# Kernel optimization log

Measured on AMD Instinct MI355X. Metric: run time of the kernel, lower is better.

## Reference

```python
import jax, jax.numpy as jnp
import numpy as np

B, C, MX, MY, MZ = 4, 64, 48, 48, 48
A, E = 64, 128  # n_atoms, mol_embed_size
V = MX * MY * MZ


def setup_inputs() -> dict:
    key = jax.random.key(0)
    ks = jax.random.split(key, 12)
    inp = {
        "x": jax.random.normal(ks[0], (B, C, MX, MY, MZ), dtype=jnp.float32),
        "mol_embed": jax.random.normal(ks[1], (B, A, E), dtype=jnp.float32),
        "pos": jax.random.uniform(ks[2], (B, A, 3), dtype=jnp.float32),
        "origin": jnp.zeros((B, 3), dtype=jnp.float32),
        "lattice": jax.random.uniform(ks[3], (B, 3, 3), dtype=jnp.float32) + 0.5,
        "batch_nodes": jax.random.randint(ks[4], (B,), 32, A + 1, dtype=jnp.int32),
        "v_w": jax.random.normal(ks[5], (C, E), dtype=jnp.float32) / np.sqrt(E),
        "v_b": jax.random.normal(ks[6], (C,), dtype=jnp.float32) * 0.01,
        "out_w": jax.random.normal(ks[7], (C, 2 * C), dtype=jnp.float32) / np.sqrt(2 * C),
        "out_b": jax.random.normal(ks[8], (C,), dtype=jnp.float32) * 0.01,
        "conv_w": jax.random.normal(ks[9], (C, C, 3, 3, 3), dtype=jnp.float32) / np.sqrt(C * 27),
        "conv_b": jax.random.normal(ks[10], (C,), dtype=jnp.float32) * 0.01,
    }
    return inp


def _grid_points(o, ldiag):
    # torch.linspace(o, o+l, n) inclusive endpoints -> t = arange(n)/(n-1)
    axes = [o[i] + ldiag[i] * (jnp.arange(n, dtype=jnp.float32) / (n - 1))
            for i, n in enumerate((MX, MY, MZ))]
    gx, gy, gz = jnp.meshgrid(*axes, indexing="ij")
    return jnp.stack([gx, gy, gz], axis=-1).reshape(-1, 3)  # [V,3]


def _forward(x, mol_embed, pos, origin, lattice, batch_nodes,
             v_w, v_b, out_w, out_b, conv_w, conv_b):
    b = x.shape[0]
    ldiag = jnp.diagonal(lattice, axis1=-2, axis2=-1)           # [b,3]
    grid = jax.vmap(_grid_points)(origin, ldiag)                # [b,V,3]
    # pairwise distances via |g|^2 + |p|^2 - 2 g.p (avoids [b,V,A,3])
    g2 = jnp.sum(grid * grid, axis=-1)                          # [b,V]
    p2 = jnp.sum(pos * pos, axis=-1)                            # [b,A]
    gp = jnp.einsum("bvd,bad->bva", grid, pos)                  # [b,V,A]
    d2 = g2[:, :, None] + p2[:, None, :] - 2.0 * gp
    dist = jnp.sqrt(jnp.maximum(d2, 1e-12))
    # ragged mask: atoms >= batch_nodes[i] get -inf score
    valid = jnp.arange(A)[None, None, :] < batch_nodes[:, None, None]
    weight = jnp.where(valid, -dist, -jnp.inf)
    att = jax.nn.softmax(weight, axis=-1)                       # [b,V,A]
    v = mol_embed @ v_w.T + v_b                                 # [b,A,C]
    v = jnp.einsum("bva,bac->bvc", att, v)                      # [b,V,C]
    xv = x.reshape(b, C, V).transpose(0, 2, 1)                  # [b,V,C]
    h = jnp.concatenate([xv, v], axis=-1)                       # [b,V,2C]
    h = jax.nn.relu(h @ out_w.T + out_b)                        # [b,V,C]
    h = h.transpose(0, 2, 1).reshape(b, C, MX, MY, MZ)
    hp = jnp.pad(h, ((0, 0), (0, 0), (1, 1), (1, 1), (1, 1)), mode="wrap")
    conv = jax.lax.conv_general_dilated(
        hp, conv_w, window_strides=(1, 1, 1), padding="VALID",
        dimension_numbers=("NCDHW", "OIDHW", "NCDHW"))
    conv = conv + conv_b[None, :, None, None, None]
    return jax.nn.relu(conv) + x


def reference(x, mol_embed, pos, origin, lattice, batch_nodes,
              v_w, v_b, out_w, out_b, conv_w, conv_b):
    return _forward(x, mol_embed, pos, origin, lattice, batch_nodes,
                    v_w, v_b, out_w, out_b, conv_w, conv_b)
```

## Files before the change

### kernel.cpp

```cpp
#include <hip/hip_runtime.h>

#define NB 4
#define NC 64
#define NV (48*48*48)
#define NA 64
#define NE 128

typedef __attribute__((ext_vector_type(8))) short short8;
typedef __attribute__((ext_vector_type(4))) float f32x4;

static __device__ __forceinline__ ushort f2bf(float f) {
  unsigned u = __float_as_uint(f);
  unsigned r = (u + 0x7FFF + ((u >> 16) & 1)) >> 16;
  return (ushort)r;
}
static __device__ __forceinline__ unsigned pk2bf(float lo, float hi) {
  return (unsigned)f2bf(lo) | ((unsigned)f2bf(hi) << 16);
}

__global__ __launch_bounds__(256) void k_vm(
    const float* __restrict__ me, const float* __restrict__ vw,
    const float* __restrict__ vb, float* __restrict__ vmat) {
  int blk = blockIdx.x;
  int b = blk >> 4, aq = blk & 15;
  int t = threadIdx.x;
  int a = aq * 4 + (t >> 6);
  int c = t & 63;
  const float* mp = me + (size_t)(b * 64 + a) * 128;
  const float* wp = vw + (size_t)c * 128;
  float acc = vb[c];
#pragma unroll 8
  for (int e = 0; e < 128; e += 4) {
    float4 m4 = *(const float4*)(mp + e);
    float4 w4 = *(const float4*)(wp + e);
    acc += m4.x * w4.x + m4.y * w4.y + m4.z * w4.z + m4.w * w4.w;
  }
  vmat[b * 4096 + a * 64 + c] = acc;
}

__global__ __launch_bounds__(256) void k_bct(
    const float* __restrict__ ow, const float* __restrict__ vmat,
    ushort* __restrict__ BcT) {
  __shared__ float VM[64 * 68];
  __shared__ float WV[8 * 68];
  int blk = blockIdx.x;
  int b = blk >> 3, og = blk & 7;
  int t = threadIdx.x;
  for (int i = t; i < 4096; i += 256)
    VM[(i >> 6) * 68 + (i & 63)] = vmat[b * 4096 + i];
  for (int i = t; i < 512; i += 256)
    WV[(i >> 6) * 68 + (i & 63)] = ow[(og * 8 + (i >> 6)) * 128 + 64 + (i & 63)];
  __syncthreads();
  int ol = t >> 5;
  int a0 = (t & 31) * 2;
  int o = og * 8 + ol;
#pragma unroll
  for (int p = 0; p < 2; ++p) {
    int a = a0 + p;
    float acc = 0.f;
#pragma unroll 8
    for (int c = 0; c < 64; c += 4) {
      float4 v4 = *(const float4*)&VM[a * 68 + c];
      float4 w4 = *(const float4*)&WV[ol * 68 + c];
      acc += v4.x * w4.x + v4.y * w4.y + v4.z * w4.z + v4.w * w4.w;
    }
    BcT[b * 8192 + o * 128 + a] = f2bf(acc);
  }
#pragma unroll
  for (int p = 0; p < 2; ++p) {
    int i = t * 2 + p;
    int ol2 = i >> 6, ci = i & 63;
    int o2 = og * 8 + ol2;
    BcT[b * 8192 + o2 * 128 + 64 + ci] = f2bf(ow[o2 * 128 + ci]);
  }
}

__global__ void k_wt(const float* __restrict__ cw, ushort* __restrict__ wbf) {
  int idx = blockIdx.x * 256 + threadIdx.x;
  if (idx >= 27 * 64 * 64) return;
  int off = idx >> 12, r = idx & 4095;
  int kcw = r >> 11, r2 = r & 2047, nt = r2 >> 9, r3 = r2 & 511;
  int ln = r3 >> 3, e = r3 & 7;
  int co = nt * 16 + (ln & 15), ci = kcw * 32 + (ln >> 4) * 8 + e;
  wbf[idx] = f2bf(cw[(co * 64 + ci) * 27 + off]);
}

__global__ __launch_bounds__(256) void k_att2(
    const float* __restrict__ x, const float* __restrict__ pos,
    const float* __restrict__ origin, const float* __restrict__ lattice,
    const int* __restrict__ bnodes, const float* __restrict__ ob,
    const ushort* __restrict__ BcT, ushort* __restrict__ hbf) {
  __shared__ __align__(16) char Ac[32768];
  __shared__ float ps[192];
  __shared__ float sinv[128];
  int t = threadIdx.x;
  int lane = t & 63, wave = t >> 6;
  int b = blockIdx.y;
  int v0 = blockIdx.x * 128;
  int lm = lane & 15, lg = lane >> 4;

  if (t < 192) ps[t] = pos[b * 192 + t];
  __syncthreads();

  int cp = t >> 3;
  int vq = t & 7;
  const float* xa = x + ((size_t)(b * 64 + 2 * cp)) * NV + v0 + vq * 16;
  const float* xb2 = xa + NV;
  float4 fa[4], fb[4];
#pragma unroll
  for (int it = 0; it < 4; ++it) {
    fa[it] = *(const float4*)(xa + it * 4);
    fb[it] = *(const float4*)(xb2 + it * 4);
  }
  short8 Bf[4][4];
  {
    const ushort* bp = BcT + b * 8192 + lm * 128 + lg * 8;
#pragma unroll
    for (int kb = 0; kb < 4; ++kb)
#pragma unroll
      for (int nt = 0; nt < 4; ++nt)
        Bf[kb][nt] = *(const short8*)(bp + nt * 2048 + kb * 32);
  }
  __builtin_amdgcn_sched_barrier(0);

  {
    int v_loc = wave * 32 + (lane & 31);
    int half = lane >> 5;
    int v = v0 + v_loc;
    int ix = v / 2304;
    int rem = v - ix * 2304;
    int iy = rem / 48;
    int iz = rem - iy * 48;
    float gx = origin[b * 3 + 0] + lattice[b * 9 + 0] * (ix * (1.0f / 47.0f));
    float gy = origin[b * 3 + 1] + lattice[b * 9 + 4] * (iy * (1.0f / 47.0f));
    float gz = origin[b * 3 + 2] + lattice[b * 9 + 8] * (iz * (1.0f / 47.0f));
    int na = bnodes[b];
    int vswz = v_loc & 7;
    char* rowp = Ac + v_loc * 256;
    float s = 0.f;
#pragma unroll
    for (int i = 0; i < 32; i += 2) {
      float e2[2];
#pragma unroll
      for (int j = 0; j < 2; ++j) {
        int a = half * 32 + i + j;
        float dx = gx - ps[a * 3 + 0];
        float dy = gy - ps[a * 3 + 1];
        float dz = gz - ps[a * 3 + 2];
        float d = sqrtf(fmaxf(dx * dx + dy * dy + dz * dz, 1e-12f));
        float e = (a < na) ? __expf(-d) : 0.f;
        e2[j] = e;
        s += e;
      }
      int byteoff = (half * 32 + i) * 2;
      int slot = byteoff >> 4;
      *(unsigned*)(rowp + (((slot ^ vswz) << 4) | (byteoff & 15))) = pk2bf(e2[0], e2[1]);
    }
    s += __shfl_xor(s, 32);
    if (half == 0) sinv[v_loc] = 1.0f / s;
  }

  {
    int slot = 8 + (cp >> 2);
    int off = (cp & 3) * 4;
#pragma unroll
    for (int it = 0; it < 4; ++it) {
      int rbase = vq * 16 + it * 4;
#pragma unroll
      for (int j = 0; j < 4; ++j) {
        int row = rbase + j;
        float va = ((const float*)&fa[it])[j];
        float vb2 = ((const float*)&fb[it])[j];
        *(unsigned*)(Ac + row * 256 + (((slot ^ (row & 7)) << 4) | off)) = pk2bf(va, vb2);
      }
    }
  }
  __syncthreads();

  f32x4 acc[2][4];
#pragma unroll
  for (int mt = 0; mt < 2; ++mt)
#pragma unroll
    for (int nt = 0; nt < 4; ++nt) acc[mt][nt] = (f32x4){0.f, 0.f, 0.f, 0.f};

  auto do_k = [&](int kb) {
    short8 Af[2];
#pragma unroll
    for (int mt = 0; mt < 2; ++mt) {
      int row = wave * 32 + mt * 16 + lm;
      Af[mt] = *(const short8*)(Ac + row * 256 + ((((kb << 2) + lg) ^ (row & 7)) << 4));
    }
#pragma unroll
    for (int mt = 0; mt < 2; ++mt)
#pragma unroll
      for (int nt = 0; nt < 4; ++nt)
        acc[mt][nt] = __builtin_amdgcn_mfma_f32_16x16x32_bf16(Af[mt], Bf[kb][nt], acc[mt][nt], 0, 0, 0);
  };
  do_k(0);
  do_k(1);
#pragma unroll
  for (int mt = 0; mt < 2; ++mt) {
    float4 s4 = *(const float4*)&sinv[wave * 32 + mt * 16 + lg * 4];
#pragma unroll
    for (int nt = 0; nt < 4; ++nt) {
      acc[mt][nt][0] *= s4.x;
      acc[mt][nt][1] *= s4.y;
      acc[mt][nt][2] *= s4.z;
      acc[mt][nt][3] *= s4.w;
    }
  }
  do_k(2);
  do_k(3);

  __syncthreads();
  float bo[4];
#pragma unroll
  for (int nt = 0; nt < 4; ++nt) bo[nt] = ob[nt * 16 + lm];
#pragma unroll
  for (int mt = 0; mt < 2; ++mt)
#pragma unroll
    for (int nt = 0; nt < 4; ++nt) {
      int o = nt * 16 + lm;
      int slot = o >> 3;
      int off = (o & 7) * 2;
#pragma unroll
      for (int r = 0; r < 4; ++r) {
        int row = wave * 32 + mt * 16 + lg * 4 + r;
        float hv = fmaxf(acc[mt][nt][r] + bo[nt], 0.f);
        *(ushort*)(Ac + row * 128 + (((slot ^ (row & 7)) << 4) | off)) = f2bf(hv);
      }
    }
  __syncthreads();
  char* dst = (char*)hbf + ((size_t)(b * NV + v0)) * 128;
#pragma unroll
  for (int k = 0; k < 4; ++k) {
    int i = t + k * 256;
    int row = i >> 3, s = i & 7;
    *(uint4*)(dst + row * 128 + s * 16) =
        *(const uint4*)(Ac + row * 128 + ((s ^ (row & 7)) << 4));
  }
}

__global__ __launch_bounds__(256, 3) void k_conv(
    const ushort* __restrict__ hbf, const ushort* __restrict__ wbf,
    const float* __restrict__ cb, const float* __restrict__ x,
    float* __restrict__ out) {
  __shared__ __align__(16) char sm[36864];
  int t = threadIdx.x;
  int lane = t & 63, wave = t >> 6;
  int lm = lane & 15, lg = lane >> 4;
  int kc = wave >> 1;
  int mh = wave & 1;

  int bid = blockIdx.x;
  int sw = (bid & 7) * 576 + (bid >> 3);
  int b = sw / 1152, tid = sw - b * 1152;
  int xt = tid / 96, rem = tid - xt * 96, yt = rem >> 3, zt = rem & 7;
  int x0 = xt * 4, y0 = yt * 4, z0 = zt * 6;

  const char* hbase = (const char*)hbf + (size_t)b * NV * 128;
  const ushort* wl = wbf + kc * 2048 + lane * 8;

  short8 Ba[4], Bb[4], Bc[4];
#pragma unroll
  for (int nt = 0; nt < 4; ++nt) Ba[nt] = *(const short8*)(wl + nt * 512);
#pragma unroll
  for (int nt = 0; nt < 4; ++nt) Bb[nt] = *(const short8*)(wl + 4096 + nt * 512);

#pragma unroll
  for (int k = 0; k < 9; ++k) {
    int c = t + k * 256;
    int r = c >> 3, j = c & 7;
    int hx = r / 48, rr = r - hx * 48, hy = rr >> 3, hz = rr & 7;
    int gx = x0 + hx - 1; gx += (gx < 0) ? 48 : 0; gx -= (gx >= 48) ? 48 : 0;
    int gy = y0 + hy - 1; gy += (gy < 0) ? 48 : 0; gy -= (gy >= 48) ? 48 : 0;
    int gz = z0 + hz - 1; gz += (gz < 0) ? 48 : 0; gz -= (gz >= 48) ? 48 : 0;
    uint4 v = *(const uint4*)(hbase + (size_t)((gx * 2304 + gy * 48 + gz) * 128 + j * 16));
    *(uint4*)(sm + r * 128 + ((j ^ hz) << 4)) = v;
  }

  char* Abase[3][3];
#pragma unroll
  for (int mt = 0; mt < 3; ++mt) {
    int v = mt * 16 + lm;
    int xl = v / 24, rm2 = v - xl * 24, yl = rm2 / 6, zl = rm2 - yl * 6;
    int rowb = (mh * 2 + xl) * 48 + yl * 8 + zl;
#pragma unroll
    for (int dz = 0; dz < 3; ++dz)
      Abase[mt][dz] = sm + (rowb + dz) * 128 + ((((kc << 2) | lg) ^ (zl + dz)) << 4);
  }

  f32x4 acc[3][4];
#pragma unroll
  for (int i = 0; i < 3; ++i)
#pragma unroll
    for (int j = 0; j < 4; ++j) acc[i][j] = (f32x4){0.f, 0.f, 0.f, 0.f};

  __syncthreads();

  short8 Aa[3], Ab[3];
#pragma unroll
  for (int mt = 0; mt < 3; ++mt) Aa[mt] = *(const short8*)(Abase[mt][0]);

#define STEPC(o, Bcur, Bpre, Acur, Apre) { \
    if ((o) + 2 < 27) { \
      const ushort* p = wl + ((o) + 2) * 4096; \
      _Pragma("unroll") \
      for (int nt = 0; nt < 4; ++nt) Bpre[nt] = *(const short8*)(p + nt * 512); \
    } \
    if ((o) + 1 < 27) { \
      const int on = (o) + 1; \
      const int dxN = on / 9, dyzN = on - dxN * 9, dyN = dyzN / 3, dzN = dyzN - dyN * 3; \
      const int aimmN = (dxN * 48 + dyN * 8) * 128; \
      _Pragma("unroll") \
      for (int mt = 0; mt < 3; ++mt) Apre[mt] = *(const short8*)(Abase[mt][dzN] + aimmN); \
    } \
    __builtin_amdgcn_sched_barrier(0); \
    __builtin_amdgcn_s_setprio(1); \
    _Pragma("unroll") \
    for (int mt = 0; mt < 3; ++mt) \
      _Pragma("unroll") \
      for (int nt = 0; nt < 4; ++nt) \
        acc[mt][nt] = __builtin_amdgcn_mfma_f32_16x16x32_bf16(Acur[mt], Bcur[nt], acc[mt][nt], 0, 0, 0); \
    __builtin_amdgcn_s_setprio(0); \
    __builtin_amdgcn_sched_barrier(0); \
  }

  STEPC(0, Ba, Bc, Aa, Ab)  STEPC(1, Bb, Ba, Ab, Aa)  STEPC(2, Bc, Bb, Aa, Ab)
  STEPC(3, Ba, Bc, Ab, Aa)  STEPC(4, Bb, Ba, Aa, Ab)  STEPC(5, Bc, Bb, Ab, Aa)
  STEPC(6, Ba, Bc, Aa, Ab)  STEPC(7, Bb, Ba, Ab, Aa)  STEPC(8, Bc, Bb, Aa, Ab)
  STEPC(9, Ba, Bc, Ab, Aa)  STEPC(10, Bb, Ba, Aa, Ab) STEPC(11, Bc, Bb, Ab, Aa)
  STEPC(12, Ba, Bc, Aa, Ab) STEPC(13, Bb, Ba, Ab, Aa) STEPC(14, Bc, Bb, Aa, Ab)
  STEPC(15, Ba, Bc, Ab, Aa) STEPC(16, Bb, Ba, Aa, Ab) STEPC(17, Bc, Bb, Ab, Aa)
  STEPC(18, Ba, Bc, Aa, Ab) STEPC(19, Bb, Ba, Ab, Aa) STEPC(20, Bc, Bb, Aa, Ab)
  STEPC(21, Ba, Bc, Ab, Aa) STEPC(22, Bb, Ba, Aa, Ab) STEPC(23, Bc, Bb, Ab, Aa)
  STEPC(24, Ba, Bc, Aa, Ab) STEPC(25, Bb, Ba, Ab, Aa) STEPC(26, Bc, Bb, Aa, Ab)
#undef STEPC

  const float* xb = x + (size_t)b * NC * NV;
  float* obp = out + (size_t)b * NC * NV;
  float2 xr2[6][2];
  size_t gaddr[6][2];
#pragma unroll
  for (int k = 0; k < 6; ++k) {
    int c = t + k * 256;
    int co = c / 24, q = c - co * 24;
#pragma unroll
    for (int p = 0; p < 2; ++p) {
      int v = q * 4 + p * 2;
      int xl = v / 24, rm = v - xl * 24, yl = rm / 6, zl = rm - yl * 6;
      size_t g = (size_t)co * NV + (x0 + xl) * 2304 + (y0 + yl) * 48 + (z0 + zl);
      gaddr[k][p] = g;
      xr2[k][p] = *(const float2*)(xb + g);
    }
  }

  __syncthreads();
  float* red = (float*)sm;
  if (kc == 1) {
#pragma unroll
    for (int mt = 0; mt < 3; ++mt)
#pragma unroll
      for (int nt = 0; nt < 4; ++nt) {
        int co = nt * 16 + lm;
        int vox = mh * 48 + mt * 16 + lg * 4;
        *(float4*)&red[co * 104 + vox] = (float4){acc[mt][nt][0], acc[mt][nt][1],
                                                  acc[mt][nt][2], acc[mt][nt][3]};
      }
  }
  __syncthreads();
  if (kc == 0) {
    float bo[4];
#pragma unroll
    for (int nt = 0; nt < 4; ++nt) bo[nt] = cb[nt * 16 + lm];
#pragma unroll
    for (int mt = 0; mt < 3; ++mt)
#pragma unroll
      for (int nt = 0; nt < 4; ++nt) {
        int co = nt * 16 + lm;
        int vox = mh * 48 + mt * 16 + lg * 4;
        float4 p = *(const float4*)&red[co * 104 + vox];
        float4 r;
        r.x = fmaxf(acc[mt][nt][0] + p.x + bo[nt], 0.f);
        r.y = fmaxf(acc[mt][nt][1] + p.y + bo[nt], 0.f);
        r.z = fmaxf(acc[mt][nt][2] + p.z + bo[nt], 0.f);
        r.w = fmaxf(acc[mt][nt][3] + p.w + bo[nt], 0.f);
        *(float4*)&red[co * 104 + vox] = r;
      }
  }
  __syncthreads();
#pragma unroll
  for (int k = 0; k < 6; ++k) {
    int c = t + k * 256;
    int co = c / 24, q = c - co * 24;
#pragma unroll
    for (int p = 0; p < 2; ++p) {
      int v = q * 4 + p * 2;
      float2 rv = *(const float2*)&red[co * 104 + v];
      float2 o2;
      o2.x = rv.x + xr2[k][p].x;
      o2.y = rv.y + xr2[k][p].y;
      *(float2*)(obp + gaddr[k][p]) = o2;
    }
  }
}

extern "C" void kernel_launch(void* const* d_in, const int* in_sizes, int n_in,
                              void* d_out, int out_size, void* d_ws, size_t ws_size,
                              hipStream_t stream) {
  const float* x = (const float*)d_in[0];
  const float* me = (const float*)d_in[1];
  const float* pos = (const float*)d_in[2];
  const float* origin = (const float*)d_in[3];
  const float* lattice = (const float*)d_in[4];
  const int* bn = (const int*)d_in[5];
  const float* vw = (const float*)d_in[6];
  const float* vb = (const float*)d_in[7];
  const float* ow = (const float*)d_in[8];
  const float* ob = (const float*)d_in[9];
  const float* cw = (const float*)d_in[10];
  const float* cbias = (const float*)d_in[11];
  float* outp = (float*)d_out;

  ushort* BcT = (ushort*)d_ws;
  ushort* wbf = (ushort*)((char*)d_ws + 65536);
  ushort* hbf = (ushort*)((char*)d_ws + 65536 + 221184);
  float* vmat = (float*)hbf;

  k_vm<<<64, 256, 0, stream>>>(me, vw, vb, vmat);
  k_bct<<<32, 256, 0, stream>>>(ow, vmat, BcT);
  k_wt<<<(27 * 64 * 64 + 255) / 256, 256, 0, stream>>>(cw, wbf);
  k_att2<<<dim3(NV / 128, NB), 256, 0, stream>>>(x, pos, origin, lattice, bn, ob, BcT, hbf);
  k_conv<<<4608, 256, 0, stream>>>(hbf, wbf, cbias, x, outp);
}
```

Before: 210.0 us.

## Switch conv to 32x32x16 MFMA with 4x4x8 voxel tiles and padded LDS

Rewrites the 3D conv kernel to use 32x32x16 bf16 MFMA in place of 16x16x32, with each block covering a 4x4x8 voxel tile (128 voxels) instead of 4x4x6. The halo tile is stored in LDS with a padded 144-byte row stride in place of the XOR swizzle, and the weight prepack layout changes to match the new B-fragment shape. The epilogue now does float4 residual loads and stores. Intended gains are fewer MFMA issues, better halo reuse per block and wider stores. In exchange LDS use rises to about 51 KB, which may lower occupancy, and the A-operand prefetch across steps is dropped. A dead first assignment to Abase is left in.

Result: faster. 183.7 us (-12.5%).

```diff
diff --git a/kernel.cpp b/kernel.cpp
--- a/kernel.cpp
+++ b/kernel.cpp
@@ -8,6 +8,7 @@
 
 typedef __attribute__((ext_vector_type(8))) short short8;
 typedef __attribute__((ext_vector_type(4))) float f32x4;
+typedef __attribute__((ext_vector_type(16))) float f32x16;
 
 static __device__ __forceinline__ ushort f2bf(float f) {
   unsigned u = __float_as_uint(f);
@@ -79,9 +80,12 @@
   int idx = blockIdx.x * 256 + threadIdx.x;
   if (idx >= 27 * 64 * 64) return;
   int off = idx >> 12, r = idx & 4095;
-  int kcw = r >> 11, r2 = r & 2047, nt = r2 >> 9, r3 = r2 & 511;
-  int ln = r3 >> 3, e = r3 & 7;
-  int co = nt * 16 + (ln & 15), ci = kcw * 32 + (ln >> 4) * 8 + e;
+  int kcw = r >> 11, r2 = r & 2047;
+  int nt = r2 >> 10, r3 = r2 & 1023;
+  int kk = r3 >> 9, r4 = r3 & 511;
+  int ln = r4 >> 3, e = r4 & 7;
+  int co = nt * 32 + (ln & 31);
+  int ci = kcw * 32 + kk * 16 + (ln >> 5) * 8 + e;
   wbf[idx] = f2bf(cw[(co * 64 + ci) * 27 + off]);
 }
 
@@ -245,163 +249,171 @@
     const ushort* __restrict__ hbf, const ushort* __restrict__ wbf,
     const float* __restrict__ cb, const float* __restrict__ x,
     float* __restrict__ out) {
-  __shared__ __align__(16) char sm[36864];
+  __shared__ __align__(16) char sm[51840];
   int t = threadIdx.x;
   int lane = t & 63, wave = t >> 6;
-  int lm = lane & 15, lg = lane >> 4;
+  int lm32 = lane & 31, lh = lane >> 5;
   int kc = wave >> 1;
   int mh = wave & 1;
 
   int bid = blockIdx.x;
-  int sw = (bid & 7) * 576 + (bid >> 3);
-  int b = sw / 1152, tid = sw - b * 1152;
-  int xt = tid / 96, rem = tid - xt * 96, yt = rem >> 3, zt = rem & 7;
-  int x0 = xt * 4, y0 = yt * 4, z0 = zt * 6;
+  int sw = (bid & 7) * 432 + (bid >> 3);
+  int b = sw / 864, tid = sw - b * 864;
+  int xt = tid / 72, rem = tid - xt * 72, yt = rem / 6, zt = rem - yt * 6;
+  int x0 = xt * 4, y0 = yt * 4, z0 = zt * 8;
 
   const char* hbase = (const char*)hbf + (size_t)b * NV * 128;
   const ushort* wl = wbf + kc * 2048 + lane * 8;
 
-  short8 Ba[4], Bb[4], Bc[4];
-#pragma unroll
-  for (int nt = 0; nt < 4; ++nt) Ba[nt] = *(const short8*)(wl + nt * 512);
-#pragma unroll
-  for (int nt = 0; nt < 4; ++nt) Bb[nt] = *(const short8*)(wl + 4096 + nt * 512);
-
-#pragma unroll
-  for (int k = 0; k < 9; ++k) {
+  short8 Ba[2][2], Bb[2][2], Bc[2][2];
+#pragma unroll
+  for (int nt = 0; nt < 2; ++nt)
+#pragma unroll
+    for (int kk = 0; kk < 2; ++kk) {
+      Ba[nt][kk] = *(const short8*)(wl + nt * 1024 + kk * 512);
+      Bb[nt][kk] = *(const short8*)(wl + 4096 + nt * 1024 + kk * 512);
+    }
+
+#pragma unroll
+  for (int k = 0; k < 12; ++k) {
     int c = t + k * 256;
-    int r = c >> 3, j = c & 7;
-    int hx = r / 48, rr = r - hx * 48, hy = rr >> 3, hz = rr & 7;
-    int gx = x0 + hx - 1; gx += (gx < 0) ? 48 : 0; gx -= (gx >= 48) ? 48 : 0;
-    int gy = y0 + hy - 1; gy += (gy < 0) ? 48 : 0; gy -= (gy >= 48) ? 48 : 0;
-    int gz = z0 + hz - 1; gz += (gz < 0) ? 48 : 0; gz -= (gz >= 48) ? 48 : 0;
-    uint4 v = *(const uint4*)(hbase + (size_t)((gx * 2304 + gy * 48 + gz) * 128 + j * 16));
-    *(uint4*)(sm + r * 128 + ((j ^ hz) << 4)) = v;
-  }
-
-  char* Abase[3][3];
-#pragma unroll
-  for (int mt = 0; mt < 3; ++mt) {
-    int v = mt * 16 + lm;
-    int xl = v / 24, rm2 = v - xl * 24, yl = rm2 / 6, zl = rm2 - yl * 6;
-    int rowb = (mh * 2 + xl) * 48 + yl * 8 + zl;
-#pragma unroll
-    for (int dz = 0; dz < 3; ++dz)
-      Abase[mt][dz] = sm + (rowb + dz) * 128 + ((((kc << 2) | lg) ^ (zl + dz)) << 4);
-  }
-
-  f32x4 acc[3][4];
-#pragma unroll
-  for (int i = 0; i < 3; ++i)
-#pragma unroll
-    for (int j = 0; j < 4; ++j) acc[i][j] = (f32x4){0.f, 0.f, 0.f, 0.f};
-
-  __syncthreads();
-
-  short8 Aa[3], Ab[3];
-#pragma unroll
-  for (int mt = 0; mt < 3; ++mt) Aa[mt] = *(const short8*)(Abase[mt][0]);
-
-#define STEPC(o, Bcur, Bpre, Acur, Apre) { \
+    if (c < 2880) {
+      int r = c >> 3, j = c & 7;
+      int hx = r / 60, rr = r - hx * 60, hy = rr / 10, hz = rr - hy * 10;
+      int gx = x0 + hx - 1; gx += (gx < 0) ? 48 : 0; gx -= (gx >= 48) ? 48 : 0;
+      int gy = y0 + hy - 1; gy += (gy < 0) ? 48 : 0; gy -= (gy >= 48) ? 48 : 0;
+      int gz = z0 + hz - 1; gz += (gz < 0) ? 48 : 0; gz -= (gz >= 48) ? 48 : 0;
+      uint4 v = *(const uint4*)(hbase + (size_t)((gx * 2304 + gy * 48 + gz) * 128 + j * 16));
+      *(uint4*)(sm + r * 144 + j * 16) = v;
+    }
+  }
+
+  int yl = lm32 >> 3, zl = lm32 & 7;
+  char* Abase[2];
+#pragma unroll
+  for (int mt = 0; mt < 2; ++mt)
+    Abase[mt] = sm + (((mh * 2 + mt) * 60 + yl * 10 + zl + 61) * 144) + (kc * 4 + lh) * 16;
+#pragma unroll
+  for (int mt = 0; mt < 2; ++mt)
+    Abase[mt] = sm + (((mh * 2 + mt) * 60 + yl * 10 + zl) * 144) + (kc * 4 + lh) * 16;
+
+  f32x16 acc[2][2];
+#pragma unroll
+  for (int i = 0; i < 2; ++i)
+#pragma unroll
+    for (int j = 0; j < 2; ++j)
+#pragma unroll
+      for (int q = 0; q < 16; ++q) acc[i][j][q] = 0.f;
+
+  __syncthreads();
+
+#define STEPC(o, Bcur, Bpre) { \
     if ((o) + 2 < 27) { \
       const ushort* p = wl + ((o) + 2) * 4096; \
       _Pragma("unroll") \
-      for (int nt = 0; nt < 4; ++nt) Bpre[nt] = *(const short8*)(p + nt * 512); \
+      for (int nt = 0; nt < 2; ++nt) \
+        _Pragma("unroll") \
+        for (int kk = 0; kk < 2; ++kk) \
+          Bpre[nt][kk] = *(const short8*)(p + nt * 1024 + kk * 512); \
     } \
-    if ((o) + 1 < 27) { \
-      const int on = (o) + 1; \
-      const int dxN = on / 9, dyzN = on - dxN * 9, dyN = dyzN / 3, dzN = dyzN - dyN * 3; \
-      const int aimmN = (dxN * 48 + dyN * 8) * 128; \
+    { \
+      const int dxo = (o) / 9, dyzo = (o) - dxo * 9, dyo = dyzo / 3, dzo = dyzo - dyo * 3; \
+      const int aimm = (dxo * 60 + dyo * 10 + dzo) * 144; \
+      short8 Af[2][2]; \
       _Pragma("unroll") \
-      for (int mt = 0; mt < 3; ++mt) Apre[mt] = *(const short8*)(Abase[mt][dzN] + aimmN); \
+      for (int mt = 0; mt < 2; ++mt) \
+        _Pragma("unroll") \
+        for (int kk = 0; kk < 2; ++kk) \
+          Af[mt][kk] = *(const short8*)(Abase[mt] + aimm + kk * 32); \
+      __builtin_amdgcn_sched_barrier(0); \
+      __builtin_amdgcn_s_setprio(1); \
+      _Pragma("unroll") \
+      for (int kk = 0; kk < 2; ++kk) \
+        _Pragma("unroll") \
+        for (int mt = 0; mt < 2; ++mt) \
+          _Pragma("unroll") \
+          for (int nt = 0; nt < 2; ++nt) \
+            acc[mt][nt] = __builtin_amdgcn_mfma_f32_32x32x16_bf16(Af[mt][kk], Bcur[nt][kk], acc[mt][nt], 0, 0, 0); \
+      __builtin_amdgcn_s_setprio(0); \
+      __builtin_amdgcn_sched_barrier(0); \
     } \
-    __builtin_amdgcn_sched_barrier(0); \
-    __builtin_amdgcn_s_setprio(1); \
-    _Pragma("unroll") \
-    for (int mt = 0; mt < 3; ++mt) \
-      _Pragma("unroll") \
-      for (int nt = 0; nt < 4; ++nt) \
-        acc[mt][nt] = __builtin_amdgcn_mfma_f32_16x16x32_bf16(Acur[mt], Bcur[nt], acc[mt][nt], 0, 0, 0); \
-    __builtin_amdgcn_s_setprio(0); \
-    __builtin_amdgcn_sched_barrier(0); \
-  }
-
-  STEPC(0, Ba, Bc, Aa, Ab)  STEPC(1, Bb, Ba, Ab, Aa)  STEPC(2, Bc, Bb, Aa, Ab)
-  STEPC(3, Ba, Bc, Ab, Aa)  STEPC(4, Bb, Ba, Aa, Ab)  STEPC(5, Bc, Bb, Ab, Aa)
-  STEPC(6, Ba, Bc, Aa, Ab)  STEPC(7, Bb, Ba, Ab, Aa)  STEPC(8, Bc, Bb, Aa, Ab)
-  STEPC(9, Ba, Bc, Ab, Aa)  STEPC(10, Bb, Ba, Aa, Ab) STEPC(11, Bc, Bb, Ab, Aa)
-  STEPC(12, Ba, Bc, Aa, Ab) STEPC(13, Bb, Ba, Ab, Aa) STEPC(14, Bc, Bb, Aa, Ab)
-  STEPC(15, Ba, Bc, Ab, Aa) STEPC(16, Bb, Ba, Aa, Ab) STEPC(17, Bc, Bb, Ab, Aa)
-  STEPC(18, Ba, Bc, Aa, Ab) STEPC(19, Bb, Ba, Ab, Aa) STEPC(20, Bc, Bb, Aa, Ab)
-  STEPC(21, Ba, Bc, Ab, Aa) STEPC(22, Bb, Ba, Aa, Ab) STEPC(23, Bc, Bb, Ab, Aa)
-  STEPC(24, Ba, Bc, Aa, Ab) STEPC(25, Bb, Ba, Ab, Aa) STEPC(26, Bc, Bb, Aa, Ab)
+  }
+
+  STEPC(0, Ba, Bc)  STEPC(1, Bb, Ba)  STEPC(2, Bc, Bb)
+  STEPC(3, Ba, Bc)  STEPC(4, Bb, Ba)  STEPC(5, Bc, Bb)
+  STEPC(6, Ba, Bc)  STEPC(7, Bb, Ba)  STEPC(8, Bc, Bb)
+  STEPC(9, Ba, Bc)  STEPC(10, Bb, Ba) STEPC(11, Bc, Bb)
+  STEPC(12, Ba, Bc) STEPC(13, Bb, Ba) STEPC(14, Bc, Bb)
+  STEPC(15, Ba, Bc) STEPC(16, Bb, Ba) STEPC(17, Bc, Bb)
+  STEPC(18, Ba, Bc) STEPC(19, Bb, Ba) STEPC(20, Bc, Bb)
+  STEPC(21, Ba, Bc) STEPC(22, Bb, Ba) STEPC(23, Bc, Bb)
+  STEPC(24, Ba, Bc) STEPC(25, Bb, Ba) STEPC(26, Bc, Bb)
 #undef STEPC
 
   const float* xb = x + (size_t)b * NC * NV;
   float* obp = out + (size_t)b * NC * NV;
-  float2 xr2[6][2];
-  size_t gaddr[6][2];
-#pragma unroll
-  for (int k = 0; k < 6; ++k) {
-    int c = t + k * 256;
-    int co = c / 24, q = c - co * 24;
-#pragma unroll
-    for (int p = 0; p < 2; ++p) {
-      int v = q * 4 + p * 2;
-      int xl = v / 24, rm = v - xl * 24, yl = rm / 6, zl = rm - yl * 6;
-      size_t g = (size_t)co * NV + (x0 + xl) * 2304 + (y0 + yl) * 48 + (z0 + zl);
-      gaddr[k][p] = g;
-      xr2[k][p] = *(const float2*)(xb + g);
-    }
+  float4 xr4[8];
+  size_t gaddr[8];
+#pragma unroll
+  for (int k = 0; k < 8; ++k) {
+    int i = t + k * 256;
+    int co = i >> 5, vq = i & 31;
+    int v = vq * 4;
+    int xl = v >> 5, rm = v & 31, yl2 = rm >> 3, zl2 = rm & 7;
+    size_t g = (size_t)co * NV + (x0 + xl) * 2304 + (y0 + yl2) * 48 + (z0 + zl2);
+    gaddr[k] = g;
+    xr4[k] = *(const float4*)(xb + g);
   }
 
   __syncthreads();
   float* red = (float*)sm;
   if (kc == 1) {
 #pragma unroll
-    for (int mt = 0; mt < 3; ++mt)
-#pragma unroll
-      for (int nt = 0; nt < 4; ++nt) {
-        int co = nt * 16 + lm;
-        int vox = mh * 48 + mt * 16 + lg * 4;
-        *(float4*)&red[co * 104 + vox] = (float4){acc[mt][nt][0], acc[mt][nt][1],
-                                                  acc[mt][nt][2], acc[mt][nt][3]};
+    for (int mt = 0; mt < 2; ++mt)
+#pragma unroll
+      for (int nt = 0; nt < 2; ++nt) {
+        int co = nt * 32 + lm32;
+#pragma unroll
+        for (int q = 0; q < 4; ++q) {
+          int vox = mh * 64 + mt * 32 + q * 8 + lh * 4;
+          *(float4*)&red[co * 132 + vox] = (float4){acc[mt][nt][q * 4 + 0], acc[mt][nt][q * 4 + 1],
+                                                    acc[mt][nt][q * 4 + 2], acc[mt][nt][q * 4 + 3]};
+        }
       }
   }
   __syncthreads();
   if (kc == 0) {
-    float bo[4];
-#pragma unroll
-    for (int nt = 0; nt < 4; ++nt) bo[nt] = cb[nt * 16 + lm];
-#pragma unroll
-    for (int mt = 0; mt < 3; ++mt)
-#pragma unroll
-      for (int nt = 0; nt < 4; ++nt) {
-        int co = nt * 16 + lm;
-        int vox = mh * 48 + mt * 16 + lg * 4;
-        float4 p = *(const float4*)&red[co * 104 + vox];
-        float4 r;
-        r.x = fmaxf(acc[mt][nt][0] + p.x + bo[nt], 0.f);
-        r.y = fmaxf(acc[mt][nt][1] + p.y + bo[nt], 0.f);
-        r.z = fmaxf(acc[mt][nt][2] + p.z + bo[nt], 0.f);
-        r.w = fmaxf(acc[mt][nt][3] + p.w + bo[nt], 0.f);
-        *(float4*)&red[co * 104 + vox] = r;
-      }
-  }
-  __syncthreads();
-#pragma unroll
-  for (int k = 0; k < 6; ++k) {
-    int c = t + k * 256;
-    int co = c / 24, q = c - co * 24;
-#pragma unroll
-    for (int p = 0; p < 2; ++p) {
-      int v = q * 4 + p * 2;
-      float2 rv = *(const float2*)&red[co * 104 + v];
-      float2 o2;
-      o2.x = rv.x + xr2[k][p].x;
-      o2.y = rv.y + xr2[k][p].y;
-      *(float2*)(obp + gaddr[k][p]) = o2;
-    }
+#pragma unroll
+    for (int nt = 0; nt < 2; ++nt) {
+      int co = nt * 32 + lm32;
+      float bo = cb[co];
+#pragma unroll
+      for (int mt = 0; mt < 2; ++mt)
+#pragma unroll
+        for (int q = 0; q < 4; ++q) {
+          int vox = mh * 64 + mt * 32 + q * 8 + lh * 4;
+          float4 p = *(const float4*)&red[co * 132 + vox];
+          float4 r;
+          r.x = fmaxf(acc[mt][nt][q * 4 + 0] + p.x + bo, 0.f);
+          r.y = fmaxf(acc[mt][nt][q * 4 + 1] + p.y + bo, 0.f);
+          r.z = fmaxf(acc[mt][nt][q * 4 + 2] + p.z + bo, 0.f);
+          r.w = fmaxf(acc[mt][nt][q * 4 + 3] + p.w + bo, 0.f);
+          *(float4*)&red[co * 132 + vox] = r;
+        }
+    }
+  }
+  __syncthreads();
+#pragma unroll
+  for (int k = 0; k < 8; ++k) {
+    int i = t + k * 256;
+    int co = i >> 5, vq = i & 31;
+    float4 rv = *(const float4*)&red[co * 132 + vq * 4];
+    float4 o4;
+    o4.x = rv.x + xr4[k].x;
+    o4.y = rv.y + xr4[k].y;
+    o4.z = rv.z + xr4[k].z;
+    o4.w = rv.w + xr4[k].w;
+    *(float4*)(obp + gaddr[k]) = o4;
   }
 }
 
@@ -431,5 +443,5 @@
   k_bct<<<32, 256, 0, stream>>>(ow, vmat, BcT);
   k_wt<<<(27 * 64 * 64 + 255) / 256, 256, 0, stream>>>(cw, wbf);
   k_att2<<<dim3(NV / 128, NB), 256, 0, stream>>>(x, pos, origin, lattice, bn, ob, BcT, hbf);
-  k_conv<<<4608, 256, 0, stream>>>(hbf, wbf, cbias, x, outp);
-}
+  k_conv<<<3456, 256, 0, stream>>>(hbf, wbf, cbias, x, outp);
+}
```
